# Kernel optimization log

Hardware: AMD Instinct MI355X
Metric: run time of the kernel (lower is better)

The kernel has to match this reference:

```python
import jax, jax.numpy as jnp
import numpy as np

# dims (match init_kwargs)
B, S, HID = 1, 2048, 2048
NH = 16            # num_attention_heads
DN = 128           # qk_nope_head_dim
DR = 64            # qk_rope_head_dim
DH = DN + DR       # qk_head_dim = 192
DV = 128           # v_head_dim
QL = 1536          # q_lora_rank
KL = 512           # kv_lora_rank
EPS = 1e-6
ROPE_THETA = 10000.0
# yarn mscale: scaling = qk_head_dim**-0.5 * m^2, m = 0.1*mscale_all_dim*ln(factor)+1
_M = 0.1 * 1.0 * float(np.log(40.0)) + 1.0
SCALING = DH ** (-0.5) * _M * _M


def setup_inputs() -> dict:
    key = jax.random.key(0)
    ks = jax.random.split(key, 8)
    hidden_states = jax.random.normal(ks[0], (B, S, HID), jnp.float32)
    # real rotary tables of width DR
    inv_freq = 1.0 / (ROPE_THETA ** (np.arange(0, DR, 2, dtype=np.float64) / DR))
    freqs = np.outer(np.arange(S, dtype=np.float64), inv_freq)      # [S, DR/2]
    emb = np.concatenate([freqs, freqs], axis=-1)                   # [S, DR]
    cos = jnp.broadcast_to(jnp.asarray(np.cos(emb), jnp.float32), (B, S, DR))
    sin = jnp.broadcast_to(jnp.asarray(np.sin(emb), jnp.float32), (B, S, DR))
    sd = 0.02
    w_qa = jax.random.normal(ks[1], (QL, HID), jnp.float32) * sd          # q_a_proj
    w_qa_ln = jnp.ones((QL,), jnp.float32)                                 # q_a_layernorm
    w_qb = jax.random.normal(ks[2], (NH * DH, QL), jnp.float32) * sd       # q_b_proj
    w_kva = jax.random.normal(ks[3], (KL + DR, HID), jnp.float32) * sd     # kv_a_proj_with_mqa
    w_kva_ln = jnp.ones((KL,), jnp.float32)                                # kv_a_layernorm
    w_kvb = jax.random.normal(ks[4], (NH * (DN + DV), KL), jnp.float32) * sd  # kv_b_proj
    w_o = jax.random.normal(ks[5], (HID, NH * DV), jnp.float32) * sd       # o_proj
    return dict(hidden_states=hidden_states, cos=cos, sin=sin, w_qa=w_qa,
                w_qa_ln=w_qa_ln, w_qb=w_qb, w_kva=w_kva, w_kva_ln=w_kva_ln,
                w_kvb=w_kvb, w_o=w_o)


def rmsnorm(x, w):
    var = jnp.mean(x * x, axis=-1, keepdims=True)
    return w * (x * jax.lax.rsqrt(var + EPS))


def rotate_half(x):
    x1, x2 = jnp.split(x, 2, axis=-1)
    return jnp.concatenate([-x2, x1], axis=-1)


def deinterleave(x):
    # view(b,h,s,d//2,2).transpose(4,3).reshape(b,h,s,d)
    b, h, s, d = x.shape
    return jnp.swapaxes(x.reshape(b, h, s, d // 2, 2), -1, -2).reshape(b, h, s, d)


def reference(hidden_states, cos, sin, w_qa, w_qa_ln, w_qb, w_kva, w_kva_ln, w_kvb, w_o):
    # --- low-rank Q path: q_a_proj -> RMSNorm -> q_b_proj ---
    q_lat = rmsnorm(jnp.einsum('bsh,qh->bsq', hidden_states, w_qa), w_qa_ln)
    q = jnp.einsum('bsq,oq->bso', q_lat, w_qb)                # [B,S,NH*DH]
    q = q.reshape(B, S, NH, DH).transpose(0, 2, 1, 3)          # [B,NH,S,DH]
    q_pass, q_rot = q[..., :DN], q[..., DN:]
    # --- compressed KV path ---
    ckv = jnp.einsum('bsh,oh->bso', hidden_states, w_kva)      # [B,S,KL+DR]
    k_lat, k_rot = ckv[..., :KL], ckv[..., KL:]
    kv = jnp.einsum('bsk,ok->bso', rmsnorm(k_lat, w_kva_ln), w_kvb)
    kv = kv.reshape(B, S, NH, DN + DV).transpose(0, 2, 1, 3)   # [B,NH,S,DN+DV]
    k_pass, v = kv[..., :DN], kv[..., DN:]
    k_rot = k_rot[:, None]                                     # [B,1,S,DR]
    # --- interleaved RoPE on the rope halves ---
    q_rot = deinterleave(q_rot)
    k_rot = deinterleave(k_rot)
    cos_u, sin_u = cos[:, None], sin[:, None]                  # [B,1,S,DR]
    q_rot = q_rot * cos_u + rotate_half(q_rot) * sin_u
    k_rot = k_rot * cos_u + rotate_half(k_rot) * sin_u
    k_rot = jnp.broadcast_to(k_rot, (B, NH, S, DR))
    # --- assemble and SDPA (causal) ---
    qq = jnp.concatenate([q_pass, q_rot], axis=-1)             # [B,NH,S,DH]
    kk = jnp.concatenate([k_pass, k_rot], axis=-1)             # [B,NH,S,DH]
    scores = jnp.einsum('bhqd,bhkd->bhqk', qq, kk) * SCALING
    causal = jnp.tril(jnp.ones((S, S), bool))
    scores = jnp.where(causal, scores, jnp.finfo(scores.dtype).min)
    attn = jax.nn.softmax(scores, axis=-1)
    out = jnp.einsum('bhqk,bhkd->bhqd', attn, v)               # [B,NH,S,DV]
    out = out.transpose(0, 2, 1, 3).reshape(B, S, NH * DV)
    return jnp.einsum('bso,ho->bsh', out, w_o)                 # o_proj -> [B,S,HID]
```

## Files before the change

### kernel.cpp

```cpp
#include <hip/hip_runtime.h>
#include <math.h>
#include <stdint.h>

typedef unsigned short u16;
typedef __attribute__((ext_vector_type(8))) short bf16x8;
typedef __attribute__((ext_vector_type(4))) float f32x4;

#define SEQ 2048
#define HIDN 2048
#define QLR 1536
#define NHEAD 16
#define DHEAD 192
#define DVAL 128
#define KLR 512
#define NCAT 2112

__device__ __forceinline__ u16 f2bf(float f) {
  union { float f; uint32_t u; } v; v.f = f;
  uint32_t r = v.u + 0x7fffu + ((v.u >> 16) & 1u);
  return (u16)(r >> 16);
}
__device__ __forceinline__ float bf2f(u16 x) {
  union { uint32_t u; float f; } v; v.u = ((uint32_t)x) << 16;
  return v.f;
}

__global__ __launch_bounds__(256) void convert_multi(
    const float* __restrict__ s0, u16* __restrict__ d0, int n0,
    const float* __restrict__ s1, u16* __restrict__ d1, int n1,
    const float* __restrict__ s2, u16* __restrict__ d2, int n2,
    const float* __restrict__ s3, u16* __restrict__ d3, int n3,
    const float* __restrict__ s4, u16* __restrict__ d4, int n4_,
    const float* __restrict__ s5, u16* __restrict__ d5, int n5) {
  const float* s; u16* d; int n4;
  switch (blockIdx.y) {
    case 0: s = s0; d = d0; n4 = n0; break;
    case 1: s = s1; d = d1; n4 = n1; break;
    case 2: s = s2; d = d2; n4 = n2; break;
    case 3: s = s3; d = d3; n4 = n3; break;
    case 4: s = s4; d = d4; n4 = n4_; break;
    default: s = s5; d = d5; n4 = n5; break;
  }
  int stride = gridDim.x * blockDim.x;
  for (int i = blockIdx.x * blockDim.x + threadIdx.x; i < n4; i += stride) {
    float4 v = reinterpret_cast<const float4*>(s)[i];
    ushort4 o;
    o.x = f2bf(v.x); o.y = f2bf(v.y); o.z = f2bf(v.z); o.w = f2bf(v.w);
    reinterpret_cast<ushort4*>(d)[i] = o;
  }
}

template<bool BF16_OUT>
__global__ __launch_bounds__(256) void gemm_bt(const u16* __restrict__ A,
                                               const u16* __restrict__ B,
                                               void* __restrict__ Cv,
                                               int M, int N, int K) {
  __shared__ __align__(16) u16 As[2][128 * 64];
  __shared__ __align__(16) u16 Bs[2][128 * 64];
  const int tid = threadIdx.x;
  const int wid = tid >> 6;
  const int lane = tid & 63;
  const int lr = lane & 15;
  const int lh = lane >> 4;
  const int wm = wid >> 1, wn = wid & 1;
  const int rowBase = blockIdx.y * 128;
  const int colBase = blockIdx.x * 128;

  f32x4 acc[4][4] = {};

  auto stage = [&](int kt, int buf) {
#pragma unroll
    for (int c = 0; c < 4; ++c) {
      const int chunk = wid * 4 + c;
      const int slin = chunk * 64 + lane;
      const int row = slin >> 3;
      const int ks = slin & 7;
      const int kcol = kt * 64 + ((ks ^ (row & 7)) << 3);
      const u16* srcA = A + (size_t)(rowBase + row) * K + kcol;
      __builtin_amdgcn_global_load_lds((const __attribute__((address_space(1))) void*)srcA,
                                       (__attribute__((address_space(3))) void*)(&As[buf][0] + chunk * 512),
                                       16, 0, 0);
      const int brow = (colBase + row < N) ? (colBase + row) : (N - 1);
      const u16* srcB = B + (size_t)brow * K + kcol;
      __builtin_amdgcn_global_load_lds((const __attribute__((address_space(1))) void*)srcB,
                                       (__attribute__((address_space(3))) void*)(&Bs[buf][0] + chunk * 512),
                                       16, 0, 0);
    }
  };

  const int nkt = K >> 6;
  stage(0, 0);
  asm volatile("s_waitcnt vmcnt(0)" ::: "memory");
  __syncthreads();

  int cur = 0;
  for (int kt = 0; kt < nkt; ++kt) {
    if (kt + 1 < nkt) stage(kt + 1, cur ^ 1);
#pragma unroll
    for (int kk = 0; kk < 2; ++kk) {
      bf16x8 af[4], bfr[4];
#pragma unroll
      for (int m = 0; m < 4; ++m) {
        int row = wm * 64 + m * 16 + lr;
        int slot = (kk * 4 + lh) ^ (row & 7);
        af[m] = *reinterpret_cast<const bf16x8*>(&As[cur][0] + row * 64 + slot * 8);
      }
#pragma unroll
      for (int n = 0; n < 4; ++n) {
        int row = wn * 64 + n * 16 + lr;
        int slot = (kk * 4 + lh) ^ (row & 7);
        bfr[n] = *reinterpret_cast<const bf16x8*>(&Bs[cur][0] + row * 64 + slot * 8);
      }
#pragma unroll
      for (int m = 0; m < 4; ++m)
#pragma unroll
        for (int n = 0; n < 4; ++n)
          acc[m][n] = __builtin_amdgcn_mfma_f32_16x16x32_bf16(af[m], bfr[n], acc[m][n], 0, 0, 0);
    }
    asm volatile("s_waitcnt vmcnt(0)" ::: "memory");
    __syncthreads();
    cur ^= 1;
  }
#pragma unroll
  for (int m = 0; m < 4; ++m) {
#pragma unroll
    for (int n = 0; n < 4; ++n) {
#pragma unroll
      for (int j = 0; j < 4; ++j) {
        int row = rowBase + wm * 64 + m * 16 + lh * 4 + j;
        int col = colBase + wn * 64 + n * 16 + lr;
        if (col < N) {
          if (BF16_OUT)
            ((u16*)Cv)[(size_t)row * N + col] = f2bf(acc[m][n][j]);
          else
            ((float*)Cv)[(size_t)row * N + col] = acc[m][n][j];
        }
      }
    }
  }
}

__global__ __launch_bounds__(256) void rmsnorm_kernel(const u16* __restrict__ in, int istride,
                                                      const float* __restrict__ w,
                                                      u16* __restrict__ out, int L, float eps) {
  int row = blockIdx.x;
  const u16* x = in + (size_t)row * istride;
  u16* o = out + (size_t)row * L;
  int tid = threadIdx.x;
  float ss = 0.f;
  for (int i = tid; i < L; i += 256) { float v = bf2f(x[i]); ss += v * v; }
#pragma unroll
  for (int off = 32; off > 0; off >>= 1) ss += __shfl_down(ss, off);
  __shared__ float red[4];
  if ((tid & 63) == 0) red[tid >> 6] = ss;
  __syncthreads();
  float tot = red[0] + red[1] + red[2] + red[3];
  float sc = rsqrtf(tot / (float)L + eps);
  for (int i = tid; i < L; i += 256) o[i] = f2bf(bf2f(x[i]) * sc * w[i]);
}

__global__ void rope_q_kernel(u16* __restrict__ qbuf, const float* __restrict__ cosb,
                              const float* __restrict__ sinb) {
  int t = blockIdx.x * blockDim.x + threadIdx.x;
  if (t >= SEQ * NHEAD) return;
  int s = t >> 4, h = t & 15;
  u16* x = qbuf + (size_t)s * (NHEAD * DHEAD) + h * DHEAD + 128;
  float xv[64];
#pragma unroll
  for (int i = 0; i < 64; ++i) xv[i] = bf2f(x[i]);
#pragma unroll
  for (int i = 0; i < 32; ++i) {
    float c = cosb[s * 64 + i], sn = sinb[s * 64 + i];
    x[i]      = f2bf(xv[2 * i] * c - xv[2 * i + 1] * sn);
    x[32 + i] = f2bf(xv[2 * i + 1] * c + xv[2 * i] * sn);
  }
}

__global__ __launch_bounds__(256) void build_k_kernel(const u16* __restrict__ kv,
                                                      const u16* __restrict__ qpre,
                                                      const float* __restrict__ cosb,
                                                      const float* __restrict__ sinb,
                                                      u16* __restrict__ Kf) {
  int s = blockIdx.x;
  int tid = threadIdx.x;
  __shared__ u16 krot[64];
  if (tid < 32) {
    float c = cosb[s * 64 + tid], sn = sinb[s * 64 + tid];
    float x0 = bf2f(qpre[(size_t)s * NCAT + 2048 + 2 * tid]);
    float x1 = bf2f(qpre[(size_t)s * NCAT + 2048 + 2 * tid + 1]);
    krot[tid]      = f2bf(x0 * c - x1 * sn);
    krot[32 + tid] = f2bf(x1 * c + x0 * sn);
  }
  __syncthreads();
  for (int idx = tid; idx < NHEAD * DHEAD; idx += 256) {
    int h = idx / DHEAD, d = idx % DHEAD;
    u16 v = (d < 128) ? kv[(size_t)s * 4096 + h * 256 + d] : krot[d - 128];
    Kf[((size_t)h * SEQ + s) * DHEAD + d] = v;
  }
}

__global__ __launch_bounds__(256) void vtrans_kernel(const u16* __restrict__ kv,
                                                     u16* __restrict__ Vt) {
  int st = blockIdx.x, dt = blockIdx.y, h = blockIdx.z;
  __shared__ u16 tile[32][33];
  int tx = threadIdx.x & 31, ty = threadIdx.x >> 5;
#pragma unroll
  for (int i = 0; i < 4; ++i) {
    int ss = st * 32 + ty + i * 8;
    tile[ty + i * 8][tx] = kv[(size_t)ss * 4096 + h * 256 + 128 + dt * 32 + tx];
  }
  __syncthreads();
#pragma unroll
  for (int i = 0; i < 4; ++i) {
    int d = dt * 32 + ty + i * 8;
    Vt[((size_t)h * DVAL + d) * SEQ + st * 32 + tx] = tile[tx][ty + i * 8];
  }
}

__global__ __launch_bounds__(256, 3) void attn_kernel(const u16* __restrict__ qbuf,
                                                      const u16* __restrict__ Kf,
                                                      const u16* __restrict__ Vt,
                                                      u16* __restrict__ attn_out,
                                                      float* __restrict__ Opart,
                                                      float* __restrict__ mlp,
                                                      float scaling) {
  const int bx = blockIdx.x;
  int h, qt, chunk;
  if (bx < 256)      { h = bx & 15;          qt = 31 - (bx >> 4);        chunk = 0; }
  else if (bx < 512) { int t = bx - 256; h = t & 15; qt = t >> 4;        chunk = 0; }
  else               { int t = bx - 512; h = t & 15; qt = 31 - (t >> 4); chunk = 1; }
  const int kt0 = chunk ? 16 : 0;
  const int kte = chunk ? qt : (qt < 15 ? qt : 15);
  const bool direct = (qt < 16);

  const int tid = threadIdx.x;
  const int wid = tid >> 6;
  const int lane = tid & 63;
  const int lr = lane & 15, lh = lane >> 4;

  __shared__ __align__(16) u16 Kl[64 * 192];
  __shared__ __align__(16) u16 Vl[144 * 64];
  __shared__ __align__(16) u16 Plds[4 * 1024];
  u16* Pw = Plds + wid * 1024;
  const int q0 = qt * 64 + wid * 16;

  for (int i = tid; i < 16 * 64; i += 256) Vl[128 * 64 + i] = 0x3F80;

  bf16x8 qf[6];
#pragma unroll
  for (int c = 0; c < 6; ++c) {
    bf16x8 q = *reinterpret_cast<const bf16x8*>(qbuf + (size_t)(q0 + lr) * (NHEAD * DHEAD) +
                                                h * DHEAD + c * 32 + lh * 8);
    bf16x8 o;
#pragma unroll
    for (int e = 0; e < 8; ++e) o[e] = (short)f2bf(bf2f((u16)q[e]) * scaling);
    qf[c] = o;
  }

  int kSrc[6], kDst[6];
#pragma unroll
  for (int i = 0; i < 6; ++i) {
    int slin = i * 256 + tid;
    int row = slin / 24;
    int ck = slin - row * 24;
    int srcck = (ck & 0x18) | ((ck & 7) ^ (row & 7));
    kSrc[i] = row * DHEAD + srcck * 8;
    kDst[i] = slin * 8;
  }
  int vSrc[4], vDst[4];
#pragma unroll
  for (int i = 0; i < 4; ++i) {
    int slin = i * 256 + tid;
    int d = slin >> 3, c = slin & 7;
    vSrc[i] = (c ^ (d & 7)) * 8;
    vDst[i] = slin * 8;
  }
  int qkOff[4][6];
#pragma unroll
  for (int f = 0; f < 4; ++f)
#pragma unroll
    for (int c = 0; c < 6; ++c) {
      int row = f * 16 + lr;
      int ckg = c * 4 + lh;
      int ck = (ckg & 0x18) | ((ckg & 7) ^ (row & 7));
      qkOff[f][c] = row * DHEAD + ck * 8;
    }
  int pvOff[9][2];
#pragma unroll
  for (int f = 0; f < 9; ++f)
#pragma unroll
    for (int kk = 0; kk < 2; ++kk) {
      int d = f * 16 + lr;
      int ckg = kk * 4 + lh;
      pvOff[f][kk] = d * 64 + ((ckg ^ (d & 7)) * 8);
    }
  int paOff[2];
#pragma unroll
  for (int kk = 0; kk < 2; ++kk) paOff[kk] = lr * 64 + (((kk * 4 + lh) ^ (lr & 7)) * 8);
  int pIdx[4][4];
#pragma unroll
  for (int f = 0; f < 4; ++f)
#pragma unroll
    for (int j = 0; j < 4; ++j) {
      int rp = lh * 4 + j;
      int col = f * 16 + lr;
      pIdx[f][j] = rp * 64 + (((col >> 3) ^ (rp & 7)) << 3) + (col & 7);
    }

  auto stageK = [&](int kt) {
    const u16* base = Kf + ((size_t)h * SEQ + kt * 64) * DHEAD;
#pragma unroll
    for (int i = 0; i < 6; ++i)
      __builtin_amdgcn_global_load_lds(
          (const __attribute__((address_space(1))) void*)(base + kSrc[i]),
          (__attribute__((address_space(3))) void*)(Kl + kDst[i]), 16, 0, 0);
  };
  auto stageV = [&](int kt) {
    const u16* base = Vt + (size_t)h * DVAL * SEQ + kt * 64;
#pragma unroll
    for (int i = 0; i < 4; ++i) {
      int d = (i * 256 + tid) >> 3;
      __builtin_amdgcn_global_load_lds(
          (const __attribute__((address_space(1))) void*)(base + (size_t)d * SEQ + vSrc[i]),
          (__attribute__((address_space(3))) void*)(Vl + vDst[i]), 16, 0, 0);
    }
  };

  float m_j[4];
  f32x4 acc[9] = {};
#pragma unroll
  for (int j = 0; j < 4; ++j) m_j[j] = -1e30f;

  stageK(kt0);
  asm volatile("s_waitcnt vmcnt(0)" ::: "memory");
  __syncthreads();

  auto do_iter = [&](int kt, bool maskTile, bool hasNextK) {
    stageV(kt);

    f32x4 sf[4] = {};
    __builtin_amdgcn_s_setprio(1);
#pragma unroll
    for (int f = 0; f < 4; ++f)
#pragma unroll
      for (int c = 0; c < 6; ++c) {
        bf16x8 kf = *reinterpret_cast<const bf16x8*>(Kl + qkOff[f][c]);
        sf[f] = __builtin_amdgcn_mfma_f32_16x16x32_bf16(qf[c], kf, sf[f], 0, 0, 0);
      }
    __builtin_amdgcn_s_setprio(0);

    __builtin_amdgcn_s_barrier();
    if (hasNextK) stageK(kt + 1);

    float mx[4];
#pragma unroll
    for (int j = 0; j < 4; ++j) mx[j] = -1e30f;
#pragma unroll
    for (int f = 0; f < 4; ++f)
#pragma unroll
      for (int j = 0; j < 4; ++j) {
        float v = sf[f][j];
        if (maskTile) {
          int kcol = kt * 64 + f * 16 + lr;
          int qrow = q0 + lh * 4 + j;
          if (kcol > qrow) v = -1e30f;
          sf[f][j] = v;
        }
        mx[j] = fmaxf(mx[j], v);
      }
#pragma unroll
    for (int off = 1; off < 16; off <<= 1)
#pragma unroll
      for (int j = 0; j < 4; ++j) mx[j] = fmaxf(mx[j], __shfl_xor(mx[j], off));

    bool need = false;
#pragma unroll
    for (int j = 0; j < 4; ++j) need |= (mx[j] > m_j[j]);
    if (__any(need)) {
      float al[4];
#pragma unroll
      for (int j = 0; j < 4; ++j) {
        float mn = fmaxf(m_j[j], mx[j]);
        al[j] = __expf(m_j[j] - mn);
        m_j[j] = mn;
      }
#pragma unroll
      for (int f = 0; f < 9; ++f)
#pragma unroll
        for (int j = 0; j < 4; ++j) acc[f][j] *= al[j];
    }
#pragma unroll
    for (int f = 0; f < 4; ++f)
#pragma unroll
      for (int j = 0; j < 4; ++j) {
        float p = __expf(sf[f][j] - m_j[j]);
        Pw[pIdx[f][j]] = f2bf(p);
      }

    if (hasNextK) asm volatile("s_waitcnt vmcnt(6)" ::: "memory");
    else          asm volatile("s_waitcnt vmcnt(0)" ::: "memory");
    __builtin_amdgcn_s_barrier();

    __builtin_amdgcn_s_setprio(1);
#pragma unroll
    for (int kk = 0; kk < 2; ++kk) {
      bf16x8 pa = *reinterpret_cast<const bf16x8*>(Pw + paOff[kk]);
#pragma unroll
      for (int f = 0; f < 9; ++f) {
        bf16x8 vb = *reinterpret_cast<const bf16x8*>(Vl + pvOff[f][kk]);
        acc[f] = __builtin_amdgcn_mfma_f32_16x16x32_bf16(pa, vb, acc[f], 0, 0, 0);
      }
    }
    __builtin_amdgcn_s_setprio(0);

    asm volatile("s_waitcnt vmcnt(0)" ::: "memory");
    __builtin_amdgcn_s_barrier();
  };

  for (int kt = kt0; kt < kte; ++kt) do_iter(kt, false, true);
  do_iter(kte, kte == qt, false);

  if (direct) {
#pragma unroll
    for (int f = 0; f < 8; ++f)
#pragma unroll
      for (int j = 0; j < 4; ++j) {
        int row = q0 + lh * 4 + j;
        float l = acc[8][j];
        attn_out[(size_t)row * (NHEAD * DVAL) + h * DVAL + f * 16 + lr] = f2bf(acc[f][j] / l);
      }
  } else {
    const int pidx = h * 16 + (qt - 16);
    float* Op = Opart + (size_t)(pidx * 2 + chunk) * 8192;
#pragma unroll
    for (int f = 0; f < 8; ++f)
#pragma unroll
      for (int j = 0; j < 4; ++j) {
        int r = wid * 16 + lh * 4 + j;
        Op[r * 128 + f * 16 + lr] = acc[f][j];
      }
    if (lr == 0) {
      float* mlb = mlp + (pidx * 2 + chunk) * 128;
#pragma unroll
      for (int j = 0; j < 4; ++j) {
        int r = wid * 16 + lh * 4 + j;
        mlb[r] = m_j[j];
        mlb[64 + r] = acc[8][j];
      }
    }
  }
}

__global__ __launch_bounds__(256) void attn_combine(const float* __restrict__ Opart,
                                                    const float* __restrict__ mlp,
                                                    u16* __restrict__ attnb) {
  const int b = blockIdx.x;
  const int h = b & 15, q2 = b >> 4;
  const int pidx = h * 16 + q2;
  const int qt = 16 + q2;
  const float* O0 = Opart + (size_t)(pidx * 2 + 0) * 8192;
  const float* O1 = Opart + (size_t)(pidx * 2 + 1) * 8192;
  const float* ml0 = mlp + (pidx * 2 + 0) * 128;
  const float* ml1 = mlp + (pidx * 2 + 1) * 128;
  __shared__ float w0s[64], w1s[64], iLs[64];
  const int tid = threadIdx.x;
  if (tid < 64) {
    float m0 = ml0[tid], l0 = ml0[64 + tid];
    float m1 = ml1[tid], l1 = ml1[64 + tid];
    float M = fmaxf(m0, m1);
    float a0 = __expf(m0 - M), a1 = __expf(m1 - M);
    w0s[tid] = a0; w1s[tid] = a1;
    iLs[tid] = 1.f / (l0 * a0 + l1 * a1);
  }
  __syncthreads();
  for (int idx = tid; idx < 8192; idx += 256) {
    int r = idx >> 7, c = idx & 127;
    float o = (O0[idx] * w0s[r] + O1[idx] * w1s[r]) * iLs[r];
    attnb[(size_t)(qt * 64 + r) * (NHEAD * DVAL) + h * DVAL + c] = f2bf(o);
  }
}

extern "C" void kernel_launch(void* const* d_in, const int* in_sizes, int n_in,
                              void* d_out, int out_size, void* d_ws, size_t ws_size,
                              hipStream_t stream) {
  const float* hidden   = (const float*)d_in[0];
  const float* cosb     = (const float*)d_in[1];
  const float* sinb     = (const float*)d_in[2];
  const float* w_qa     = (const float*)d_in[3];
  const float* w_qa_ln  = (const float*)d_in[4];
  const float* w_qb     = (const float*)d_in[5];
  const float* w_kva    = (const float*)d_in[6];
  const float* w_kva_ln = (const float*)d_in[7];
  const float* w_kvb    = (const float*)d_in[8];
  const float* w_o      = (const float*)d_in[9];
  float* out = (float*)d_out;

  char* ws = (char*)d_ws;
  size_t off = 0;
  auto alloc = [&](size_t bytes) -> char* {
    char* p = ws + off;
    off = (off + bytes + 255) & ~(size_t)255;
    return p;
  };
  u16* hbf    = (u16*)alloc((size_t)SEQ * HIDN * 2);
  u16* wcat   = (u16*)alloc((size_t)NCAT * HIDN * 2);
  u16* wqbbf  = (u16*)alloc((size_t)(NHEAD * DHEAD) * QLR * 2);
  u16* wkvbbf = (u16*)alloc((size_t)4096 * KLR * 2);
  u16* wobf   = (u16*)alloc((size_t)HIDN * HIDN * 2);
  u16* qpre   = (u16*)alloc((size_t)SEQ * NCAT * 2);
  u16* qlat   = (u16*)alloc((size_t)SEQ * QLR * 2);
  u16* qbuf   = (u16*)alloc((size_t)SEQ * NHEAD * DHEAD * 2);
  u16* klat   = (u16*)alloc((size_t)SEQ * KLR * 2);
  u16* kvbuf  = (u16*)alloc((size_t)SEQ * 4096 * 2);
  u16* Kf     = (u16*)alloc((size_t)NHEAD * SEQ * DHEAD * 2);
  u16* Vt     = (u16*)alloc((size_t)NHEAD * DVAL * SEQ * 2);
  u16* attnb  = (u16*)alloc((size_t)SEQ * NHEAD * DVAL * 2);
  (void)ws_size; (void)n_in; (void)in_sizes; (void)out_size;

  float* Opart = (float*)ws;
  float* mlp   = (float*)(ws + (size_t)512 * 8192 * 4);

  convert_multi<<<dim3(128, 6), 256, 0, stream>>>(
      hidden, hbf, SEQ * HIDN / 4,
      w_qa, wcat, QLR * HIDN / 4,
      w_kva, wcat + (size_t)QLR * HIDN, 576 * HIDN / 4,
      w_qb, wqbbf, NHEAD * DHEAD * QLR / 4,
      w_kvb, wkvbbf, 4096 * KLR / 4,
      w_o, wobf, HIDN * HIDN / 4);

  gemm_bt<true><<<dim3(17, SEQ / 128), 256, 0, stream>>>(hbf, wcat, qpre, SEQ, NCAT, HIDN);
  rmsnorm_kernel<<<SEQ, 256, 0, stream>>>(qpre, NCAT, w_qa_ln, qlat, QLR, 1e-6f);
  gemm_bt<true><<<dim3((NHEAD * DHEAD) / 128, SEQ / 128), 256, 0, stream>>>(qlat, wqbbf, qbuf, SEQ, NHEAD * DHEAD, QLR);
  rmsnorm_kernel<<<SEQ, 256, 0, stream>>>(qpre + QLR, NCAT, w_kva_ln, klat, KLR, 1e-6f);
  gemm_bt<true><<<dim3(4096 / 128, SEQ / 128), 256, 0, stream>>>(klat, wkvbbf, kvbuf, SEQ, 4096, KLR);

  rope_q_kernel<<<(SEQ * NHEAD) / 256, 256, 0, stream>>>(qbuf, cosb, sinb);
  build_k_kernel<<<SEQ, 256, 0, stream>>>(kvbuf, qpre, cosb, sinb, Kf);
  vtrans_kernel<<<dim3(SEQ / 32, DVAL / 32, NHEAD), 256, 0, stream>>>(kvbuf, Vt);

  double Mm = 0.1 * log(40.0) + 1.0;
  float scaling = (float)(pow((double)DHEAD, -0.5) * Mm * Mm);
  attn_kernel<<<dim3(768), 256, 0, stream>>>(qbuf, Kf, Vt, attnb, Opart, mlp, scaling);
  attn_combine<<<dim3(256), 256, 0, stream>>>(Opart, mlp, attnb);

  gemm_bt<false><<<dim3(HIDN / 128, SEQ / 128), 256, 0, stream>>>(attnb, wobf, out, SEQ, HIDN, HIDN);
}
```

Before: 224.6 us.

## Split causal attention KV range into 8-tile chunks with multi-way combine

```diff
diff --git a/kernel.cpp b/kernel.cpp
--- a/kernel.cpp
+++ b/kernel.cpp
@@ -225,13 +225,16 @@
                                                       float* __restrict__ mlp,
                                                       float scaling) {
   const int bx = blockIdx.x;
-  int h, qt, chunk;
-  if (bx < 256)      { h = bx & 15;          qt = 31 - (bx >> 4);        chunk = 0; }
-  else if (bx < 512) { int t = bx - 256; h = t & 15; qt = t >> 4;        chunk = 0; }
-  else               { int t = bx - 512; h = t & 15; qt = 31 - (t >> 4); chunk = 1; }
-  const int kt0 = chunk ? 16 : 0;
-  const int kte = chunk ? qt : (qt < 15 ? qt : 15);
-  const bool direct = (qt < 16);
+  const int h = bx & 15;
+  const int s = 79 - (bx >> 4);
+  int qt, chunk;
+  if (s < 8)       { qt = s;                   chunk = 0; }
+  else if (s < 24) { qt = 8 + ((s - 8) >> 1);  chunk = (s - 8) & 1; }
+  else if (s < 48) { qt = 16 + (s - 24) / 3;   chunk = (s - 24) % 3; }
+  else             { qt = 24 + ((s - 48) >> 2); chunk = (s - 48) & 3; }
+  const int kt0 = chunk * 8;
+  const int kte = (kt0 + 7 < qt) ? (kt0 + 7) : qt;
+  const bool direct = (qt < 8);
 
   const int tid = threadIdx.x;
   const int wid = tid >> 6;
@@ -430,8 +433,8 @@
         attn_out[(size_t)row * (NHEAD * DVAL) + h * DVAL + f * 16 + lr] = f2bf(acc[f][j] / l);
       }
   } else {
-    const int pidx = h * 16 + (qt - 16);
-    float* Op = Opart + (size_t)(pidx * 2 + chunk) * 8192;
+    const int pidx = (h * 24 + (qt - 8)) * 4 + chunk;
+    float* Op = Opart + (size_t)pidx * 8192;
 #pragma unroll
     for (int f = 0; f < 8; ++f)
 #pragma unroll
@@ -440,7 +443,7 @@
         Op[r * 128 + f * 16 + lr] = acc[f][j];
       }
     if (lr == 0) {
-      float* mlb = mlp + (pidx * 2 + chunk) * 128;
+      float* mlb = mlp + pidx * 128;
 #pragma unroll
       for (int j = 0; j < 4; ++j) {
         int r = wid * 16 + lh * 4 + j;
@@ -456,26 +459,33 @@
                                                     u16* __restrict__ attnb) {
   const int b = blockIdx.x;
   const int h = b & 15, q2 = b >> 4;
-  const int pidx = h * 16 + q2;
-  const int qt = 16 + q2;
-  const float* O0 = Opart + (size_t)(pidx * 2 + 0) * 8192;
-  const float* O1 = Opart + (size_t)(pidx * 2 + 1) * 8192;
-  const float* ml0 = mlp + (pidx * 2 + 0) * 128;
-  const float* ml1 = mlp + (pidx * 2 + 1) * 128;
-  __shared__ float w0s[64], w1s[64], iLs[64];
+  const int qt = 8 + q2;
+  const int nc = (qt + 8) / 8;
+  const int pbase = (h * 24 + q2) * 4;
+  __shared__ float wgt[4][64], iLs[64];
   const int tid = threadIdx.x;
   if (tid < 64) {
-    float m0 = ml0[tid], l0 = ml0[64 + tid];
-    float m1 = ml1[tid], l1 = ml1[64 + tid];
-    float M = fmaxf(m0, m1);
-    float a0 = __expf(m0 - M), a1 = __expf(m1 - M);
-    w0s[tid] = a0; w1s[tid] = a1;
-    iLs[tid] = 1.f / (l0 * a0 + l1 * a1);
+    float m[4], l[4];
+    float M = -1e30f;
+    for (int c = 0; c < nc; ++c) {
+      m[c] = mlp[(pbase + c) * 128 + tid];
+      l[c] = mlp[(pbase + c) * 128 + 64 + tid];
+      M = fmaxf(M, m[c]);
+    }
+    float L = 0.f;
+    for (int c = 0; c < nc; ++c) {
+      float a = __expf(m[c] - M);
+      wgt[c][tid] = a;
+      L += l[c] * a;
+    }
+    iLs[tid] = 1.f / L;
   }
   __syncthreads();
   for (int idx = tid; idx < 8192; idx += 256) {
     int r = idx >> 7, c = idx & 127;
-    float o = (O0[idx] * w0s[r] + O1[idx] * w1s[r]) * iLs[r];
+    float o = 0.f;
+    for (int k = 0; k < nc; ++k) o += Opart[(size_t)(pbase + k) * 8192 + idx] * wgt[k][r];
+    o *= iLs[r];
     attnb[(size_t)(qt * 64 + r) * (NHEAD * DVAL) + h * DVAL + c] = f2bf(o);
   }
 }
@@ -506,19 +516,19 @@
   u16* wcat   = (u16*)alloc((size_t)NCAT * HIDN * 2);
   u16* wqbbf  = (u16*)alloc((size_t)(NHEAD * DHEAD) * QLR * 2);
   u16* wkvbbf = (u16*)alloc((size_t)4096 * KLR * 2);
-  u16* wobf   = (u16*)alloc((size_t)HIDN * HIDN * 2);
   u16* qpre   = (u16*)alloc((size_t)SEQ * NCAT * 2);
   u16* qlat   = (u16*)alloc((size_t)SEQ * QLR * 2);
-  u16* qbuf   = (u16*)alloc((size_t)SEQ * NHEAD * DHEAD * 2);
   u16* klat   = (u16*)alloc((size_t)SEQ * KLR * 2);
   u16* kvbuf  = (u16*)alloc((size_t)SEQ * 4096 * 2);
+  u16* wobf   = (u16*)alloc((size_t)HIDN * HIDN * 2);
+  u16* qbuf   = (u16*)alloc((size_t)SEQ * NHEAD * DHEAD * 2);
   u16* Kf     = (u16*)alloc((size_t)NHEAD * SEQ * DHEAD * 2);
   u16* Vt     = (u16*)alloc((size_t)NHEAD * DVAL * SEQ * 2);
   u16* attnb  = (u16*)alloc((size_t)SEQ * NHEAD * DVAL * 2);
   (void)ws_size; (void)n_in; (void)in_sizes; (void)out_size;
 
   float* Opart = (float*)ws;
-  float* mlp   = (float*)(ws + (size_t)512 * 8192 * 4);
+  float* mlp   = (float*)(ws + (size_t)1536 * 8192 * 4);
 
   convert_multi<<<dim3(128, 6), 256, 0, stream>>>(
       hidden, hbf, SEQ * HIDN / 4,
@@ -540,8 +550,8 @@
 
   double Mm = 0.1 * log(40.0) + 1.0;
   float scaling = (float)(pow((double)DHEAD, -0.5) * Mm * Mm);
-  attn_kernel<<<dim3(768), 256, 0, stream>>>(qbuf, Kf, Vt, attnb, Opart, mlp, scaling);
-  attn_combine<<<dim3(256), 256, 0, stream>>>(Opart, mlp, attnb);
+  attn_kernel<<<dim3(1280), 256, 0, stream>>>(qbuf, Kf, Vt, attnb, Opart, mlp, scaling);
+  attn_combine<<<dim3(384), 256, 0, stream>>>(Opart, mlp, attnb);
 
   gemm_bt<false><<<dim3(HIDN / 128, SEQ / 128), 256, 0, stream>>>(attnb, wobf, out, SEQ, HIDN, HIDN);
 }
```

New measurement: 267.7 us. 1.19x slower.

## Merge pre-attention kernels into fewer launches and overlap weight conversion with GEMM

Applied to the files above, without the earlier changes.

```diff
diff --git a/kernel.cpp b/kernel.cpp
--- a/kernel.cpp
+++ b/kernel.cpp
@@ -25,46 +25,40 @@
   return v.f;
 }
 
-__global__ __launch_bounds__(256) void convert_multi(
+__device__ __forceinline__ void conv_span(const float* __restrict__ s, u16* __restrict__ d,
+                                          int n4, int start, int stride) {
+  for (int i = start; i < n4; i += stride) {
+    float4 v = reinterpret_cast<const float4*>(s)[i];
+    ushort4 o;
+    o.x = f2bf(v.x); o.y = f2bf(v.y); o.z = f2bf(v.z); o.w = f2bf(v.w);
+    reinterpret_cast<ushort4*>(d)[i] = o;
+  }
+}
+
+__global__ __launch_bounds__(256) void convert3(
     const float* __restrict__ s0, u16* __restrict__ d0, int n0,
     const float* __restrict__ s1, u16* __restrict__ d1, int n1,
-    const float* __restrict__ s2, u16* __restrict__ d2, int n2,
-    const float* __restrict__ s3, u16* __restrict__ d3, int n3,
-    const float* __restrict__ s4, u16* __restrict__ d4, int n4_,
-    const float* __restrict__ s5, u16* __restrict__ d5, int n5) {
+    const float* __restrict__ s2, u16* __restrict__ d2, int n2) {
   const float* s; u16* d; int n4;
   switch (blockIdx.y) {
     case 0: s = s0; d = d0; n4 = n0; break;
     case 1: s = s1; d = d1; n4 = n1; break;
-    case 2: s = s2; d = d2; n4 = n2; break;
-    case 3: s = s3; d = d3; n4 = n3; break;
-    case 4: s = s4; d = d4; n4 = n4_; break;
-    default: s = s5; d = d5; n4 = n5; break;
-  }
-  int stride = gridDim.x * blockDim.x;
-  for (int i = blockIdx.x * blockDim.x + threadIdx.x; i < n4; i += stride) {
-    float4 v = reinterpret_cast<const float4*>(s)[i];
-    ushort4 o;
-    o.x = f2bf(v.x); o.y = f2bf(v.y); o.z = f2bf(v.z); o.w = f2bf(v.w);
-    reinterpret_cast<ushort4*>(d)[i] = o;
-  }
+    default: s = s2; d = d2; n4 = n2; break;
+  }
+  conv_span(s, d, n4, blockIdx.x * blockDim.x + threadIdx.x, gridDim.x * blockDim.x);
 }
 
 template<bool BF16_OUT>
-__global__ __launch_bounds__(256) void gemm_bt(const u16* __restrict__ A,
-                                               const u16* __restrict__ B,
-                                               void* __restrict__ Cv,
-                                               int M, int N, int K) {
-  __shared__ __align__(16) u16 As[2][128 * 64];
-  __shared__ __align__(16) u16 Bs[2][128 * 64];
+__device__ __forceinline__ void gemm_core(u16* __restrict__ As, u16* __restrict__ Bs,
+                                          const u16* __restrict__ A, const u16* __restrict__ B,
+                                          void* __restrict__ Cv, int N, int K,
+                                          int rowBase, int colBase) {
   const int tid = threadIdx.x;
   const int wid = tid >> 6;
   const int lane = tid & 63;
   const int lr = lane & 15;
   const int lh = lane >> 4;
   const int wm = wid >> 1, wn = wid & 1;
-  const int rowBase = blockIdx.y * 128;
-  const int colBase = blockIdx.x * 128;
 
   f32x4 acc[4][4] = {};
 
@@ -78,12 +72,12 @@
       const int kcol = kt * 64 + ((ks ^ (row & 7)) << 3);
       const u16* srcA = A + (size_t)(rowBase + row) * K + kcol;
       __builtin_amdgcn_global_load_lds((const __attribute__((address_space(1))) void*)srcA,
-                                       (__attribute__((address_space(3))) void*)(&As[buf][0] + chunk * 512),
+                                       (__attribute__((address_space(3))) void*)(As + buf * 8192 + chunk * 512),
                                        16, 0, 0);
       const int brow = (colBase + row < N) ? (colBase + row) : (N - 1);
       const u16* srcB = B + (size_t)brow * K + kcol;
       __builtin_amdgcn_global_load_lds((const __attribute__((address_space(1))) void*)srcB,
-                                       (__attribute__((address_space(3))) void*)(&Bs[buf][0] + chunk * 512),
+                                       (__attribute__((address_space(3))) void*)(Bs + buf * 8192 + chunk * 512),
                                        16, 0, 0);
     }
   };
@@ -103,13 +97,13 @@
       for (int m = 0; m < 4; ++m) {
         int row = wm * 64 + m * 16 + lr;
         int slot = (kk * 4 + lh) ^ (row & 7);
-        af[m] = *reinterpret_cast<const bf16x8*>(&As[cur][0] + row * 64 + slot * 8);
+        af[m] = *reinterpret_cast<const bf16x8*>(As + cur * 8192 + row * 64 + slot * 8);
       }
 #pragma unroll
       for (int n = 0; n < 4; ++n) {
         int row = wn * 64 + n * 16 + lr;
         int slot = (kk * 4 + lh) ^ (row & 7);
-        bfr[n] = *reinterpret_cast<const bf16x8*>(&Bs[cur][0] + row * 64 + slot * 8);
+        bfr[n] = *reinterpret_cast<const bf16x8*>(Bs + cur * 8192 + row * 64 + slot * 8);
       }
 #pragma unroll
       for (int m = 0; m < 4; ++m)
@@ -140,12 +134,60 @@
   }
 }
 
-__global__ __launch_bounds__(256) void rmsnorm_kernel(const u16* __restrict__ in, int istride,
-                                                      const float* __restrict__ w,
-                                                      u16* __restrict__ out, int L, float eps) {
-  int row = blockIdx.x;
-  const u16* x = in + (size_t)row * istride;
-  u16* o = out + (size_t)row * L;
+template<bool BF16_OUT>
+__global__ __launch_bounds__(256) void gemm_bt(const u16* __restrict__ A,
+                                               const u16* __restrict__ B,
+                                               void* __restrict__ Cv,
+                                               int M, int N, int K) {
+  __shared__ __align__(16) u16 As[2 * 8192];
+  __shared__ __align__(16) u16 Bs[2 * 8192];
+  gemm_core<BF16_OUT>(As, Bs, A, B, Cv, N, K, blockIdx.y * 128, blockIdx.x * 128);
+}
+
+__global__ __launch_bounds__(256) void gemm_qakva_conv(
+    const u16* __restrict__ hbf, const u16* __restrict__ wcat, u16* __restrict__ qpre,
+    const float* __restrict__ s0, u16* __restrict__ d0, int n0,
+    const float* __restrict__ s1, u16* __restrict__ d1, int n1,
+    const float* __restrict__ s2, u16* __restrict__ d2, int n2) {
+  __shared__ __align__(16) u16 As[2 * 8192];
+  __shared__ __align__(16) u16 Bs[2 * 8192];
+  const int bx = blockIdx.x;
+  if (bx < 272) {
+    gemm_core<true>(As, Bs, hbf, wcat, qpre, NCAT, HIDN, (bx / 17) * 128, (bx % 17) * 128);
+  } else {
+    const int t = bx - 272;
+    const int seg = t >> 6, lb = t & 63;
+    const float* s; u16* d; int n4;
+    if (seg == 0)      { s = s0; d = d0; n4 = n0; }
+    else if (seg == 1) { s = s1; d = d1; n4 = n1; }
+    else               { s = s2; d = d2; n4 = n2; }
+    conv_span(s, d, n4, lb * 256 + threadIdx.x, 64 * 256);
+  }
+}
+
+__global__ __launch_bounds__(256) void gemm_dual(
+    const u16* __restrict__ A0, const u16* __restrict__ B0, u16* __restrict__ C0,
+    const u16* __restrict__ A1, const u16* __restrict__ B1, u16* __restrict__ C1) {
+  __shared__ __align__(16) u16 As[2 * 8192];
+  __shared__ __align__(16) u16 Bs[2 * 8192];
+  const int bx = blockIdx.x;
+  if (bx < 384) {
+    gemm_core<true>(As, Bs, A0, B0, C0, NHEAD * DHEAD, QLR, (bx / 24) * 128, (bx % 24) * 128);
+  } else {
+    const int t = bx - 384;
+    gemm_core<true>(As, Bs, A1, B1, C1, 4096, KLR, (t / 32) * 128, (t % 32) * 128);
+  }
+}
+
+__global__ __launch_bounds__(256) void rmsnorm2_kernel(const u16* __restrict__ qpre,
+                                                       const float* __restrict__ wq,
+                                                       u16* __restrict__ qlat,
+                                                       const float* __restrict__ wk,
+                                                       u16* __restrict__ klat) {
+  const int row = blockIdx.x;
+  const u16* x; u16* o; const float* w; int L;
+  if (blockIdx.y == 0) { x = qpre + (size_t)row * NCAT;       w = wq; o = qlat + (size_t)row * QLR; L = QLR; }
+  else                 { x = qpre + (size_t)row * NCAT + QLR; w = wk; o = klat + (size_t)row * KLR; L = KLR; }
   int tid = threadIdx.x;
   float ss = 0.f;
   for (int i = tid; i < L; i += 256) { float v = bf2f(x[i]); ss += v * v; }
@@ -155,65 +197,65 @@
   if ((tid & 63) == 0) red[tid >> 6] = ss;
   __syncthreads();
   float tot = red[0] + red[1] + red[2] + red[3];
-  float sc = rsqrtf(tot / (float)L + eps);
+  float sc = rsqrtf(tot / (float)L + 1e-6f);
   for (int i = tid; i < L; i += 256) o[i] = f2bf(bf2f(x[i]) * sc * w[i]);
 }
 
-__global__ void rope_q_kernel(u16* __restrict__ qbuf, const float* __restrict__ cosb,
-                              const float* __restrict__ sinb) {
-  int t = blockIdx.x * blockDim.x + threadIdx.x;
-  if (t >= SEQ * NHEAD) return;
-  int s = t >> 4, h = t & 15;
-  u16* x = qbuf + (size_t)s * (NHEAD * DHEAD) + h * DHEAD + 128;
-  float xv[64];
-#pragma unroll
-  for (int i = 0; i < 64; ++i) xv[i] = bf2f(x[i]);
-#pragma unroll
-  for (int i = 0; i < 32; ++i) {
-    float c = cosb[s * 64 + i], sn = sinb[s * 64 + i];
-    x[i]      = f2bf(xv[2 * i] * c - xv[2 * i + 1] * sn);
-    x[32 + i] = f2bf(xv[2 * i + 1] * c + xv[2 * i] * sn);
-  }
-}
-
-__global__ __launch_bounds__(256) void build_k_kernel(const u16* __restrict__ kv,
-                                                      const u16* __restrict__ qpre,
-                                                      const float* __restrict__ cosb,
-                                                      const float* __restrict__ sinb,
-                                                      u16* __restrict__ Kf) {
-  int s = blockIdx.x;
-  int tid = threadIdx.x;
-  __shared__ u16 krot[64];
-  if (tid < 32) {
-    float c = cosb[s * 64 + tid], sn = sinb[s * 64 + tid];
-    float x0 = bf2f(qpre[(size_t)s * NCAT + 2048 + 2 * tid]);
-    float x1 = bf2f(qpre[(size_t)s * NCAT + 2048 + 2 * tid + 1]);
-    krot[tid]      = f2bf(x0 * c - x1 * sn);
-    krot[32 + tid] = f2bf(x1 * c + x0 * sn);
-  }
-  __syncthreads();
-  for (int idx = tid; idx < NHEAD * DHEAD; idx += 256) {
-    int h = idx / DHEAD, d = idx % DHEAD;
-    u16 v = (d < 128) ? kv[(size_t)s * 4096 + h * 256 + d] : krot[d - 128];
-    Kf[((size_t)h * SEQ + s) * DHEAD + d] = v;
-  }
-}
-
-__global__ __launch_bounds__(256) void vtrans_kernel(const u16* __restrict__ kv,
-                                                     u16* __restrict__ Vt) {
-  int st = blockIdx.x, dt = blockIdx.y, h = blockIdx.z;
-  __shared__ u16 tile[32][33];
-  int tx = threadIdx.x & 31, ty = threadIdx.x >> 5;
-#pragma unroll
-  for (int i = 0; i < 4; ++i) {
-    int ss = st * 32 + ty + i * 8;
-    tile[ty + i * 8][tx] = kv[(size_t)ss * 4096 + h * 256 + 128 + dt * 32 + tx];
-  }
-  __syncthreads();
-#pragma unroll
-  for (int i = 0; i < 4; ++i) {
-    int d = dt * 32 + ty + i * 8;
-    Vt[((size_t)h * DVAL + d) * SEQ + st * 32 + tx] = tile[tx][ty + i * 8];
+__global__ __launch_bounds__(256) void prep_kernel(u16* __restrict__ qbuf,
+                                                   const u16* __restrict__ kvbuf,
+                                                   const u16* __restrict__ qpre,
+                                                   const float* __restrict__ cosb,
+                                                   const float* __restrict__ sinb,
+                                                   u16* __restrict__ Kf,
+                                                   u16* __restrict__ Vt) {
+  __shared__ u16 sh[32 * 33];
+  const int bx = blockIdx.x;
+  const int tid = threadIdx.x;
+  if (bx < 128) {
+    int t = bx * 256 + tid;
+    int s = t >> 4, h = t & 15;
+    u16* x = qbuf + (size_t)s * (NHEAD * DHEAD) + h * DHEAD + 128;
+    float xv[64];
+#pragma unroll
+    for (int i = 0; i < 64; ++i) xv[i] = bf2f(x[i]);
+#pragma unroll
+    for (int i = 0; i < 32; ++i) {
+      float c = cosb[s * 64 + i], sn = sinb[s * 64 + i];
+      x[i]      = f2bf(xv[2 * i] * c - xv[2 * i + 1] * sn);
+      x[32 + i] = f2bf(xv[2 * i + 1] * c + xv[2 * i] * sn);
+    }
+  } else if (bx < 128 + 2048) {
+    int s = bx - 128;
+    u16* krot = sh;
+    if (tid < 32) {
+      float c = cosb[s * 64 + tid], sn = sinb[s * 64 + tid];
+      float x0 = bf2f(qpre[(size_t)s * NCAT + 2048 + 2 * tid]);
+      float x1 = bf2f(qpre[(size_t)s * NCAT + 2048 + 2 * tid + 1]);
+      krot[tid]      = f2bf(x0 * c - x1 * sn);
+      krot[32 + tid] = f2bf(x1 * c + x0 * sn);
+    }
+    __syncthreads();
+    for (int idx = tid; idx < NHEAD * DHEAD; idx += 256) {
+      int h = idx / DHEAD, d = idx % DHEAD;
+      u16 v = (d < 128) ? kvbuf[(size_t)s * 4096 + h * 256 + d] : krot[d - 128];
+      Kf[((size_t)h * SEQ + s) * DHEAD + d] = v;
+    }
+  } else {
+    int t = bx - 2176;
+    int st = t & 63, dt = (t >> 6) & 3, h = t >> 8;
+    u16 (*tile)[33] = (u16 (*)[33])sh;
+    int tx = tid & 31, ty = tid >> 5;
+#pragma unroll
+    for (int i = 0; i < 4; ++i) {
+      int ss = st * 32 + ty + i * 8;
+      tile[ty + i * 8][tx] = kvbuf[(size_t)ss * 4096 + h * 256 + 128 + dt * 32 + tx];
+    }
+    __syncthreads();
+#pragma unroll
+    for (int i = 0; i < 4; ++i) {
+      int d = dt * 32 + ty + i * 8;
+      Vt[((size_t)h * DVAL + d) * SEQ + st * 32 + tx] = tile[tx][ty + i * 8];
+    }
   }
 }
 
@@ -506,12 +548,12 @@
   u16* wcat   = (u16*)alloc((size_t)NCAT * HIDN * 2);
   u16* wqbbf  = (u16*)alloc((size_t)(NHEAD * DHEAD) * QLR * 2);
   u16* wkvbbf = (u16*)alloc((size_t)4096 * KLR * 2);
-  u16* wobf   = (u16*)alloc((size_t)HIDN * HIDN * 2);
   u16* qpre   = (u16*)alloc((size_t)SEQ * NCAT * 2);
   u16* qlat   = (u16*)alloc((size_t)SEQ * QLR * 2);
-  u16* qbuf   = (u16*)alloc((size_t)SEQ * NHEAD * DHEAD * 2);
   u16* klat   = (u16*)alloc((size_t)SEQ * KLR * 2);
   u16* kvbuf  = (u16*)alloc((size_t)SEQ * 4096 * 2);
+  u16* wobf   = (u16*)alloc((size_t)HIDN * HIDN * 2);
+  u16* qbuf   = (u16*)alloc((size_t)SEQ * NHEAD * DHEAD * 2);
   u16* Kf     = (u16*)alloc((size_t)NHEAD * SEQ * DHEAD * 2);
   u16* Vt     = (u16*)alloc((size_t)NHEAD * DVAL * SEQ * 2);
   u16* attnb  = (u16*)alloc((size_t)SEQ * NHEAD * DVAL * 2);
@@ -520,23 +562,22 @@
   float* Opart = (float*)ws;
   float* mlp   = (float*)(ws + (size_t)512 * 8192 * 4);
 
-  convert_multi<<<dim3(128, 6), 256, 0, stream>>>(
+  convert3<<<dim3(128, 3), 256, 0, stream>>>(
       hidden, hbf, SEQ * HIDN / 4,
       w_qa, wcat, QLR * HIDN / 4,
-      w_kva, wcat + (size_t)QLR * HIDN, 576 * HIDN / 4,
+      w_kva, wcat + (size_t)QLR * HIDN, 576 * HIDN / 4);
+
+  gemm_qakva_conv<<<dim3(464), 256, 0, stream>>>(
+      hbf, wcat, qpre,
       w_qb, wqbbf, NHEAD * DHEAD * QLR / 4,
       w_kvb, wkvbbf, 4096 * KLR / 4,
       w_o, wobf, HIDN * HIDN / 4);
 
-  gemm_bt<true><<<dim3(17, SEQ / 128), 256, 0, stream>>>(hbf, wcat, qpre, SEQ, NCAT, HIDN);
-  rmsnorm_kernel<<<SEQ, 256, 0, stream>>>(qpre, NCAT, w_qa_ln, qlat, QLR, 1e-6f);
-  gemm_bt<true><<<dim3((NHEAD * DHEAD) / 128, SEQ / 128), 256, 0, stream>>>(qlat, wqbbf, qbuf, SEQ, NHEAD * DHEAD, QLR);
-  rmsnorm_kernel<<<SEQ, 256, 0, stream>>>(qpre + QLR, NCAT, w_kva_ln, klat, KLR, 1e-6f);
-  gemm_bt<true><<<dim3(4096 / 128, SEQ / 128), 256, 0, stream>>>(klat, wkvbbf, kvbuf, SEQ, 4096, KLR);
-
-  rope_q_kernel<<<(SEQ * NHEAD) / 256, 256, 0, stream>>>(qbuf, cosb, sinb);
-  build_k_kernel<<<SEQ, 256, 0, stream>>>(kvbuf, qpre, cosb, sinb, Kf);
-  vtrans_kernel<<<dim3(SEQ / 32, DVAL / 32, NHEAD), 256, 0, stream>>>(kvbuf, Vt);
+  rmsnorm2_kernel<<<dim3(SEQ, 2), 256, 0, stream>>>(qpre, w_qa_ln, qlat, w_kva_ln, klat);
+
+  gemm_dual<<<dim3(896), 256, 0, stream>>>(qlat, wqbbf, qbuf, klat, wkvbbf, kvbuf);
+
+  prep_kernel<<<dim3(6272), 256, 0, stream>>>(qbuf, kvbuf, qpre, cosb, sinb, Kf, Vt);
 
   double Mm = 0.1 * log(40.0) + 1.0;
   float scaling = (float)(pow((double)DHEAD, -0.5) * Mm * Mm);
```

After: 249.1 us. 10.9% more time.

## Merge norm and prep kernels into fewer launches and relax attention barriers

Applied to the files above, without the earlier changes.

```diff
diff --git a/kernel.cpp b/kernel.cpp
--- a/kernel.cpp
+++ b/kernel.cpp
@@ -140,12 +140,15 @@
   }
 }
 
-__global__ __launch_bounds__(256) void rmsnorm_kernel(const u16* __restrict__ in, int istride,
-                                                      const float* __restrict__ w,
-                                                      u16* __restrict__ out, int L, float eps) {
-  int row = blockIdx.x;
-  const u16* x = in + (size_t)row * istride;
-  u16* o = out + (size_t)row * L;
+__global__ __launch_bounds__(256) void rmsnorm2_kernel(const u16* __restrict__ qpre,
+                                                       const float* __restrict__ wq,
+                                                       u16* __restrict__ qlat,
+                                                       const float* __restrict__ wk,
+                                                       u16* __restrict__ klat) {
+  const int row = blockIdx.x;
+  const u16* x; u16* o; const float* w; int L;
+  if (blockIdx.y == 0) { x = qpre + (size_t)row * NCAT;       w = wq; o = qlat + (size_t)row * QLR; L = QLR; }
+  else                 { x = qpre + (size_t)row * NCAT + QLR; w = wk; o = klat + (size_t)row * KLR; L = KLR; }
   int tid = threadIdx.x;
   float ss = 0.f;
   for (int i = tid; i < L; i += 256) { float v = bf2f(x[i]); ss += v * v; }
@@ -155,65 +158,65 @@
   if ((tid & 63) == 0) red[tid >> 6] = ss;
   __syncthreads();
   float tot = red[0] + red[1] + red[2] + red[3];
-  float sc = rsqrtf(tot / (float)L + eps);
+  float sc = rsqrtf(tot / (float)L + 1e-6f);
   for (int i = tid; i < L; i += 256) o[i] = f2bf(bf2f(x[i]) * sc * w[i]);
 }
 
-__global__ void rope_q_kernel(u16* __restrict__ qbuf, const float* __restrict__ cosb,
-                              const float* __restrict__ sinb) {
-  int t = blockIdx.x * blockDim.x + threadIdx.x;
-  if (t >= SEQ * NHEAD) return;
-  int s = t >> 4, h = t & 15;
-  u16* x = qbuf + (size_t)s * (NHEAD * DHEAD) + h * DHEAD + 128;
-  float xv[64];
-#pragma unroll
-  for (int i = 0; i < 64; ++i) xv[i] = bf2f(x[i]);
-#pragma unroll
-  for (int i = 0; i < 32; ++i) {
-    float c = cosb[s * 64 + i], sn = sinb[s * 64 + i];
-    x[i]      = f2bf(xv[2 * i] * c - xv[2 * i + 1] * sn);
-    x[32 + i] = f2bf(xv[2 * i + 1] * c + xv[2 * i] * sn);
-  }
-}
-
-__global__ __launch_bounds__(256) void build_k_kernel(const u16* __restrict__ kv,
-                                                      const u16* __restrict__ qpre,
-                                                      const float* __restrict__ cosb,
-                                                      const float* __restrict__ sinb,
-                                                      u16* __restrict__ Kf) {
-  int s = blockIdx.x;
-  int tid = threadIdx.x;
-  __shared__ u16 krot[64];
-  if (tid < 32) {
-    float c = cosb[s * 64 + tid], sn = sinb[s * 64 + tid];
-    float x0 = bf2f(qpre[(size_t)s * NCAT + 2048 + 2 * tid]);
-    float x1 = bf2f(qpre[(size_t)s * NCAT + 2048 + 2 * tid + 1]);
-    krot[tid]      = f2bf(x0 * c - x1 * sn);
-    krot[32 + tid] = f2bf(x1 * c + x0 * sn);
-  }
-  __syncthreads();
-  for (int idx = tid; idx < NHEAD * DHEAD; idx += 256) {
-    int h = idx / DHEAD, d = idx % DHEAD;
-    u16 v = (d < 128) ? kv[(size_t)s * 4096 + h * 256 + d] : krot[d - 128];
-    Kf[((size_t)h * SEQ + s) * DHEAD + d] = v;
-  }
-}
-
-__global__ __launch_bounds__(256) void vtrans_kernel(const u16* __restrict__ kv,
-                                                     u16* __restrict__ Vt) {
-  int st = blockIdx.x, dt = blockIdx.y, h = blockIdx.z;
-  __shared__ u16 tile[32][33];
-  int tx = threadIdx.x & 31, ty = threadIdx.x >> 5;
-#pragma unroll
-  for (int i = 0; i < 4; ++i) {
-    int ss = st * 32 + ty + i * 8;
-    tile[ty + i * 8][tx] = kv[(size_t)ss * 4096 + h * 256 + 128 + dt * 32 + tx];
-  }
-  __syncthreads();
-#pragma unroll
-  for (int i = 0; i < 4; ++i) {
-    int d = dt * 32 + ty + i * 8;
-    Vt[((size_t)h * DVAL + d) * SEQ + st * 32 + tx] = tile[tx][ty + i * 8];
+__global__ __launch_bounds__(256) void prep_kernel(u16* __restrict__ qbuf,
+                                                   const u16* __restrict__ kvbuf,
+                                                   const u16* __restrict__ qpre,
+                                                   const float* __restrict__ cosb,
+                                                   const float* __restrict__ sinb,
+                                                   u16* __restrict__ Kf,
+                                                   u16* __restrict__ Vt) {
+  __shared__ u16 sh[32 * 33];
+  const int bx = blockIdx.x;
+  const int tid = threadIdx.x;
+  if (bx < 128) {
+    int t = bx * 256 + tid;
+    int s = t >> 4, h = t & 15;
+    u16* x = qbuf + (size_t)s * (NHEAD * DHEAD) + h * DHEAD + 128;
+    float xv[64];
+#pragma unroll
+    for (int i = 0; i < 64; ++i) xv[i] = bf2f(x[i]);
+#pragma unroll
+    for (int i = 0; i < 32; ++i) {
+      float c = cosb[s * 64 + i], sn = sinb[s * 64 + i];
+      x[i]      = f2bf(xv[2 * i] * c - xv[2 * i + 1] * sn);
+      x[32 + i] = f2bf(xv[2 * i + 1] * c + xv[2 * i] * sn);
+    }
+  } else if (bx < 128 + 2048) {
+    int s = bx - 128;
+    u16* krot = sh;
+    if (tid < 32) {
+      float c = cosb[s * 64 + tid], sn = sinb[s * 64 + tid];
+      float x0 = bf2f(qpre[(size_t)s * NCAT + 2048 + 2 * tid]);
+      float x1 = bf2f(qpre[(size_t)s * NCAT + 2048 + 2 * tid + 1]);
+      krot[tid]      = f2bf(x0 * c - x1 * sn);
+      krot[32 + tid] = f2bf(x1 * c + x0 * sn);
+    }
+    __syncthreads();
+    for (int idx = tid; idx < NHEAD * DHEAD; idx += 256) {
+      int h = idx / DHEAD, d = idx % DHEAD;
+      u16 v = (d < 128) ? kvbuf[(size_t)s * 4096 + h * 256 + d] : krot[d - 128];
+      Kf[((size_t)h * SEQ + s) * DHEAD + d] = v;
+    }
+  } else {
+    int t = bx - 2176;
+    int st = t & 63, dt = (t >> 6) & 3, h = t >> 8;
+    u16 (*tile)[33] = (u16 (*)[33])sh;
+    int tx = tid & 31, ty = tid >> 5;
+#pragma unroll
+    for (int i = 0; i < 4; ++i) {
+      int ss = st * 32 + ty + i * 8;
+      tile[ty + i * 8][tx] = kvbuf[(size_t)ss * 4096 + h * 256 + 128 + dt * 32 + tx];
+    }
+    __syncthreads();
+#pragma unroll
+    for (int i = 0; i < 4; ++i) {
+      int d = dt * 32 + ty + i * 8;
+      Vt[((size_t)h * DVAL + d) * SEQ + st * 32 + tx] = tile[tx][ty + i * 8];
+    }
   }
 }
 
@@ -338,6 +341,9 @@
   auto do_iter = [&](int kt, bool maskTile, bool hasNextK) {
     stageV(kt);
 
+    asm volatile("s_waitcnt vmcnt(4)" ::: "memory");
+    __builtin_amdgcn_s_barrier();
+
     f32x4 sf[4] = {};
     __builtin_amdgcn_s_setprio(1);
 #pragma unroll
@@ -413,8 +419,7 @@
     }
     __builtin_amdgcn_s_setprio(0);
 
-    asm volatile("s_waitcnt vmcnt(0)" ::: "memory");
-    __builtin_amdgcn_s_barrier();
+    if (hasNextK) __builtin_amdgcn_s_barrier();
   };
 
   for (int kt = kt0; kt < kte; ++kt) do_iter(kt, false, true);
@@ -506,12 +511,12 @@
   u16* wcat   = (u16*)alloc((size_t)NCAT * HIDN * 2);
   u16* wqbbf  = (u16*)alloc((size_t)(NHEAD * DHEAD) * QLR * 2);
   u16* wkvbbf = (u16*)alloc((size_t)4096 * KLR * 2);
-  u16* wobf   = (u16*)alloc((size_t)HIDN * HIDN * 2);
   u16* qpre   = (u16*)alloc((size_t)SEQ * NCAT * 2);
   u16* qlat   = (u16*)alloc((size_t)SEQ * QLR * 2);
-  u16* qbuf   = (u16*)alloc((size_t)SEQ * NHEAD * DHEAD * 2);
   u16* klat   = (u16*)alloc((size_t)SEQ * KLR * 2);
   u16* kvbuf  = (u16*)alloc((size_t)SEQ * 4096 * 2);
+  u16* wobf   = (u16*)alloc((size_t)HIDN * HIDN * 2);
+  u16* qbuf   = (u16*)alloc((size_t)SEQ * NHEAD * DHEAD * 2);
   u16* Kf     = (u16*)alloc((size_t)NHEAD * SEQ * DHEAD * 2);
   u16* Vt     = (u16*)alloc((size_t)NHEAD * DVAL * SEQ * 2);
   u16* attnb  = (u16*)alloc((size_t)SEQ * NHEAD * DVAL * 2);
@@ -529,14 +534,11 @@
       w_o, wobf, HIDN * HIDN / 4);
 
   gemm_bt<true><<<dim3(17, SEQ / 128), 256, 0, stream>>>(hbf, wcat, qpre, SEQ, NCAT, HIDN);
-  rmsnorm_kernel<<<SEQ, 256, 0, stream>>>(qpre, NCAT, w_qa_ln, qlat, QLR, 1e-6f);
+  rmsnorm2_kernel<<<dim3(SEQ, 2), 256, 0, stream>>>(qpre, w_qa_ln, qlat, w_kva_ln, klat);
   gemm_bt<true><<<dim3((NHEAD * DHEAD) / 128, SEQ / 128), 256, 0, stream>>>(qlat, wqbbf, qbuf, SEQ, NHEAD * DHEAD, QLR);
-  rmsnorm_kernel<<<SEQ, 256, 0, stream>>>(qpre + QLR, NCAT, w_kva_ln, klat, KLR, 1e-6f);
   gemm_bt<true><<<dim3(4096 / 128, SEQ / 128), 256, 0, stream>>>(klat, wkvbbf, kvbuf, SEQ, 4096, KLR);
 
-  rope_q_kernel<<<(SEQ * NHEAD) / 256, 256, 0, stream>>>(qbuf, cosb, sinb);
-  build_k_kernel<<<SEQ, 256, 0, stream>>>(kvbuf, qpre, cosb, sinb, Kf);
-  vtrans_kernel<<<dim3(SEQ / 32, DVAL / 32, NHEAD), 256, 0, stream>>>(kvbuf, Vt);
+  prep_kernel<<<dim3(6272), 256, 0, stream>>>(qbuf, kvbuf, qpre, cosb, sinb, Kf, Vt);
 
   double Mm = 0.1 * log(40.0) + 1.0;
   float scaling = (float)(pow((double)DHEAD, -0.5) * Mm * Mm);
```

Result: faster. 216.0 us (-3.8%).
